# Performance work log

Hardware: AMD Instinct MI355X
Metric: run time of the kernel (lower is better)

Reference implementation:

```python
import jax, jax.numpy as jnp
import numpy as np
import math

V = 50000; E = 300; H = 512; T = 11; P = 18; L = 2048
NHEAD = 2; NLAYERS = 2; NUM_LSTM_LAYERS = 2; FF = E  # TransformerEncoderLayer dim_feedforward=embedding_dim
START, STOP = 0, 1
NEG = -10000.0


def _mk_lstm_params(key, in_dim, hid):
    ks = jax.random.split(key, 4)
    s = 1.0 / math.sqrt(hid)
    return {
        'Wi': jax.random.uniform(ks[0], (4 * hid, in_dim), minval=-s, maxval=s),
        'Wh': jax.random.uniform(ks[1], (4 * hid, hid), minval=-s, maxval=s),
        'bi': jax.random.uniform(ks[2], (4 * hid,), minval=-s, maxval=s),
        'bh': jax.random.uniform(ks[3], (4 * hid,), minval=-s, maxval=s),
    }


def setup_inputs() -> dict:
    key = jax.random.key(0)
    ks = jax.random.split(key, 32)
    sentence = jax.random.randint(ks[0], (L,), 0, V)
    pos_tagging = jax.random.randint(ks[1], (L,), 0, P)
    tf_idf = jax.random.uniform(ks[2], (L,))
    tags = jax.random.randint(ks[3], (L,), 2, T)  # avoid START/STOP as gold tags

    word_embeds = jax.random.normal(ks[4], (V, E)) * 0.1

    in_dim = E + P + 1
    half = H // 2
    lstm = []
    ki = 5
    for layer in range(NUM_LSTM_LAYERS):
        d = in_dim if layer == 0 else H
        lstm.append({'fwd': _mk_lstm_params(ks[ki], d, half), 'bwd': _mk_lstm_params(ks[ki + 1], d, half)})
        ki += 2
    h0 = jax.random.normal(ks[ki], (2 * NUM_LSTM_LAYERS, half)); ki += 1
    c0 = jax.random.normal(ks[ki], (2 * NUM_LSTM_LAYERS, half)); ki += 1

    def dense(k, o, i):
        s = 1.0 / math.sqrt(i)
        k1, k2 = jax.random.split(k)
        return (jax.random.uniform(k1, (o, i), minval=-s, maxval=s),
                jax.random.uniform(k2, (o,), minval=-s, maxval=s))

    tlayers = []
    for _ in range(NLAYERS):
        kk = jax.random.split(ks[ki], 8); ki += 1
        Wqkv, bqkv = dense(kk[0], 3 * H, H)
        Wo, bo = dense(kk[1], H, H)
        W1, b1 = dense(kk[2], FF, H)
        W2, b2 = dense(kk[3], H, FF)
        tlayers.append({
            'Wqkv': Wqkv, 'bqkv': bqkv, 'Wo': Wo, 'bo': bo,
            'W1': W1, 'b1': b1, 'W2': W2, 'b2': b2,
            'g1': jnp.ones((H,)), 'be1': jnp.zeros((H,)),
            'g2': jnp.ones((H,)), 'be2': jnp.zeros((H,)),
        })

    W_tag, b_tag = dense(ks[ki], T, H); ki += 1
    transitions = jax.random.normal(ks[ki], (T, T))
    transitions = transitions.at[START, :].set(NEG).at[:, STOP].set(NEG)

    # flatten transformer params into named entries
    inp = {
        'sentence': sentence, 'pos_tagging': pos_tagging, 'tf_idf': tf_idf, 'tags': tags,
        'word_embeds': word_embeds, 'h0': h0, 'c0': c0,
        'W_tag': W_tag, 'b_tag': b_tag, 'transitions': transitions,
    }
    for li in range(NUM_LSTM_LAYERS):
        for d in ('fwd', 'bwd'):
            for p in ('Wi', 'Wh', 'bi', 'bh'):
                inp[f'lstm{li}_{d}_{p}'] = lstm[li][d][p]
    for li in range(NLAYERS):
        for p, v in tlayers[li].items():
            inp[f't{li}_{p}'] = v
    return inp


def _lstm_dir(x, p, h0, c0, reverse):
    # x: [L, in_dim]
    def step(carry, xt):
        h, c = carry
        g = p['Wi'] @ xt + p['bi'] + p['Wh'] @ h + p['bh']
        i, f, gg, o = jnp.split(g, 4)
        i = jax.nn.sigmoid(i); f = jax.nn.sigmoid(f); o = jax.nn.sigmoid(o)
        c = f * c + i * jnp.tanh(gg)
        h = o * jnp.tanh(c)
        return (h, c), h
    _, hs = jax.lax.scan(step, (h0, c0), x, reverse=reverse)
    return hs  # [L, hid]


def _layernorm(x, g, b):
    m = jnp.mean(x, -1, keepdims=True)
    v = jnp.var(x, -1, keepdims=True)
    return (x - m) / jnp.sqrt(v + 1e-5) * g + b


def _pos_encoding(d_model, max_len):
    position = jnp.arange(max_len, dtype=jnp.float32)[:, None]
    div = jnp.exp(jnp.arange(0, d_model, 2, dtype=jnp.float32) * (-math.log(10000.0) / d_model))
    pe = jnp.zeros((max_len, d_model))
    pe = pe.at[:, 0::2].set(jnp.sin(position * div))
    pe = pe.at[:, 1::2].set(jnp.cos(position * div))
    return pe


def _encoder_layer(x, p, mask):
    # x: [L, H]; post-norm, relu FFN (PyTorch defaults), dropout=eval off
    Lx = x.shape[0]
    qkv = x @ p['Wqkv'].T + p['bqkv']
    q, k, v = jnp.split(qkv, 3, axis=-1)
    dh = H // NHEAD
    q = q.reshape(Lx, NHEAD, dh).transpose(1, 0, 2)
    k = k.reshape(Lx, NHEAD, dh).transpose(1, 0, 2)
    v = v.reshape(Lx, NHEAD, dh).transpose(1, 0, 2)
    scores = jnp.einsum('hqd,hkd->hqk', q, k) / math.sqrt(dh) + mask[None]
    attn = jax.nn.softmax(scores, axis=-1)
    o = jnp.einsum('hqk,hkd->hqd', attn, v).transpose(1, 0, 2).reshape(Lx, H)
    o = o @ p['Wo'].T + p['bo']
    x = _layernorm(x + o, p['g1'], p['be1'])
    ff = jax.nn.relu(x @ p['W1'].T + p['b1']) @ p['W2'].T + p['b2']
    return _layernorm(x + ff, p['g2'], p['be2'])


def _crf_forward(feats, transitions):
    # feats: [L, T]
    init = jnp.full((T,), NEG).at[START].set(0.0)
    def step(fv, feat):
        # next_tag_var[next, prev] = fv[prev] + trans[next, prev] + feat[next]
        m = fv[None, :] + transitions + feat[:, None]
        return jax.nn.logsumexp(m, axis=1), None
    fv, _ = jax.lax.scan(step, init, feats)
    return jax.nn.logsumexp(fv + transitions[STOP])


def _gold_score(feats, tags, transitions):
    ext = jnp.concatenate([jnp.array([START]), tags])
    Lx = feats.shape[0]
    emit = feats[jnp.arange(Lx), ext[1:]].sum()
    trans = transitions[ext[1:], ext[:-1]].sum()
    return emit + trans + transitions[STOP, ext[-1]]


def _forward_feats(sentence, pos_tagging, tf_idf, params):
    Lx = sentence.shape[0]
    embeds = params['word_embeds'][sentence]
    pos = jax.nn.one_hot(pos_tagging, P)
    x = jnp.concatenate([embeds, pos, tf_idf[:, None]], axis=1)  # [L, E+P+1]
    for li in range(NUM_LSTM_LAYERS):
        pf = {k: params[f'lstm{li}_fwd_{k}'] for k in ('Wi', 'Wh', 'bi', 'bh')}
        pb = {k: params[f'lstm{li}_bwd_{k}'] for k in ('Wi', 'Wh', 'bi', 'bh')}
        hf = _lstm_dir(x, pf, params['h0'][2 * li], params['c0'][2 * li], False)
        hb = _lstm_dir(x, pb, params['h0'][2 * li + 1], params['c0'][2 * li + 1], True)
        x = jnp.concatenate([hf, hb], axis=-1)  # [L, H]
    lstm_out = x
    src = lstm_out * math.sqrt(H) + _pos_encoding(H, Lx)
    mask = jnp.where(jnp.tril(jnp.ones((Lx, Lx), bool)), 0.0, -jnp.inf)
    for li in range(NLAYERS):
        p = {k: params[f't{li}_{k}'] for k in ('Wqkv', 'bqkv', 'Wo', 'bo', 'W1', 'b1', 'W2', 'b2', 'g1', 'be1', 'g2', 'be2')}
        src = _encoder_layer(src, p, mask)
    return src @ params['W_tag'].T + params['b_tag']  # [L, T]


def reference(sentence, pos_tagging, tf_idf, tags, word_embeds, h0, c0, W_tag, b_tag, transitions, **params):
    params = dict(params, word_embeds=word_embeds, h0=h0, c0=c0, W_tag=W_tag, b_tag=b_tag)
    feats = _forward_feats(sentence, pos_tagging, tf_idf, params)
    fwd = _crf_forward(feats, transitions)
    gold = _gold_score(feats, tags, transitions)
    return fwd - gold  # neg_log_likelihood scalar
```

## Files before the change

### kernel.cpp

```cpp
#include <hip/hip_runtime.h>
#include <math.h>

typedef unsigned short u16;
typedef unsigned int u32;
typedef _Float16 f16;
typedef f16 f16x2 __attribute__((ext_vector_type(2)));
typedef f16 f16x8 __attribute__((ext_vector_type(8)));
typedef short short8 __attribute__((ext_vector_type(8)));
typedef float f32x4 __attribute__((ext_vector_type(4)));

#define LSEQ 2048
#define NTAG 11

static __device__ __forceinline__ float b2f(u16 u){ union{u32 i; float f;} v; v.i=((u32)u)<<16; return v.f; }
static __device__ __forceinline__ u16 f2b(float f){ union{float fl; u32 i;} v; v.fl=f; u32 r=v.i+0x7fffu+((v.i>>16)&1u); return (u16)(r>>16); }
static u16 h_f2b(float f){ union{float fl; u32 i;} v; v.fl=f; u32 r=v.i+0x7fffu+((v.i>>16)&1u); return (u16)(r>>16); }
static __device__ __forceinline__ float tanh_f(float x){ float e=__expf(2.f*x); return 1.f - 2.f/(e+1.f); }
static __device__ __forceinline__ int dot4(u32 a, u32 b, int c){
#if __has_builtin(__builtin_amdgcn_sdot4)
  return __builtin_amdgcn_sdot4((int)a, (int)b, c, false);
#else
  int r = c;
  #pragma unroll
  for (int i=0;i<4;i++){
    int ai = (int)(a << (24-8*i)) >> 24;
    int bi = (int)(b << (24-8*i)) >> 24;
    r += ai*bi;
  }
  return r;
#endif
}

__global__ __launch_bounds__(256) void cvt2d_k(const float* __restrict__ src, u16* __restrict__ dst,
                                               int rows, int cols, int sld, int dld){
  int i = blockIdx.x*256 + threadIdx.x;
  if (i >= rows*dld) return;
  int r = i/dld, c = i - r*dld;
  float v = (c < cols) ? src[(long)r*sld + c] : 0.f;
  dst[i] = f2b(v);
}

__global__ __launch_bounds__(256) void whq_k(const float* __restrict__ wh,
                                             signed char* __restrict__ wq, float* __restrict__ srow){
  int row = blockIdx.x, j = threadIdx.x;
  float w = wh[row*256 + j];
  float a = fabsf(w);
  __shared__ float rm[4];
  int lane = j&63, wv = j>>6;
  #pragma unroll
  for (int o=32;o;o>>=1) a = fmaxf(a, __shfl_xor(a,o));
  if (!lane) rm[wv] = a;
  __syncthreads();
  float mx = fmaxf(fmaxf(rm[0],rm[1]),fmaxf(rm[2],rm[3]));
  float s = (mx > 0.f) ? mx*(1.f/127.f) : 1.f;
  int q = (int)rintf(w/s);
  q = q>127?127:(q<-127?-127:q);
  wq[((long)(j>>4)*1024 + row)*16 + (j&15)] = (signed char)q;
  if (j==0) srow[row] = s;
}

__global__ __launch_bounds__(256) void bsum_k(float* __restrict__ out,
    const float* bi0, const float* bh0, const float* bi1, const float* bh1,
    const float* bi2, const float* bh2, const float* bi3, const float* bh3){
  int i = blockIdx.x*256 + threadIdx.x;
  if (i >= 4096) return;
  int c = i>>10, j = i&1023;
  const float* bi = c==0?bi0:c==1?bi1:c==2?bi2:bi3;
  const float* bh = c==0?bh0:c==1?bh1:c==2?bh2:bh3;
  out[i] = bi[j] + bh[j];
}

__global__ void embed_k(const int* __restrict__ sent, const int* __restrict__ pos,
                        const float* __restrict__ tfidf, const float* __restrict__ we,
                        u16* __restrict__ x0h){
  int t = blockIdx.x, c = threadIdx.x;
  float v;
  if (c < 300)      v = we[(long)sent[t]*300 + c];
  else if (c < 318) v = (pos[t] == (c-300)) ? 1.f : 0.f;
  else if (c == 318) v = tfidf[t];
  else               v = 0.f;
  x0h[t*320 + c] = f2b(v);
}

__global__ __launch_bounds__(256) void gemm_k(const u16* __restrict__ A, const u16* __restrict__ B, void* __restrict__ C,
    int M, int N, int K, int lda, int ldb, int ldc,
    long aBS, long bBS, long cBS,
    const float* __restrict__ bias, int flags, int Npad)
{
  int zb = blockIdx.z;
  const u16* Ab = A + (long)zb*aBS;
  const u16* Bb = B + (long)zb*bBS;
  int m0 = blockIdx.y*64, n0 = blockIdx.x*64;
  __shared__ u16 As[64][40], Bs[64][40];
  int tid = threadIdx.x;
  int lane = tid & 63, wv = tid >> 6;
  int srow = tid >> 2, schk = tid & 3;
  int wr = wv >> 1, wc = wv & 1;
  int frow = lane & 15, fk = (lane >> 4) * 8;
  const u16* pa = Ab + (long)(m0+srow)*lda + schk*8;
  bool bval = (n0 + srow) < N;
  const u16* pb = Bb + (long)(n0+srow)*ldb + schk*8;
  f32x4 acc[2][2];
  #pragma unroll
  for (int mi=0;mi<2;mi++)
  #pragma unroll
  for (int ni=0;ni<2;ni++) acc[mi][ni] = (f32x4){0.f,0.f,0.f,0.f};

  for (int k0=0; k0<K; k0+=32){
    uint4 av = *(const uint4*)pa; pa += 32;
    uint4 bv; if (bval) bv = *(const uint4*)pb; else { bv.x=0u; bv.y=0u; bv.z=0u; bv.w=0u; }
    pb += 32;
    *(uint4*)&As[srow][schk*8] = av;
    *(uint4*)&Bs[srow][schk*8] = bv;
    __syncthreads();
    short8 a[2], b[2];
    a[0] = *(const short8*)&As[wr*32      + frow][fk];
    a[1] = *(const short8*)&As[wr*32 + 16 + frow][fk];
    b[0] = *(const short8*)&Bs[wc*32      + frow][fk];
    b[1] = *(const short8*)&Bs[wc*32 + 16 + frow][fk];
    #pragma unroll
    for (int mi=0;mi<2;mi++)
    #pragma unroll
    for (int ni=0;ni<2;ni++)
      acc[mi][ni] = __builtin_amdgcn_mfma_f32_16x16x32_bf16(a[mi], b[ni], acc[mi][ni], 0,0,0);
    __syncthreads();
  }
  int mrow = (lane>>4)*4, ncol = lane&15;
  #pragma unroll
  for (int mi=0;mi<2;mi++)
  #pragma unroll
  for (int ni=0;ni<2;ni++){
    int nn = n0 + wc*32 + ni*16 + ncol;
    #pragma unroll
    for (int j=0;j<4;j++){
      int mm = m0 + wr*32 + mi*16 + mrow + j;
      long ci = (long)zb*cBS + (long)mm*ldc + nn;
      if (nn < N){
        float v = acc[mi][ni][j];
        if (flags & 1) v += bias[nn];
        if (flags & 2) v = fmaxf(v, 0.f);
        if (flags & 4) ((u16*)C)[ci] = f2b(v); else ((float*)C)[ci] = v;
      } else if (nn < Npad){
        if (flags & 4) ((u16*)C)[ci] = 0; else ((float*)C)[ci] = 0.f;
      }
    }
  }
}

__global__ __launch_bounds__(1024) void lstm_r(
    const float* __restrict__ preF, const float* __restrict__ preB,
    const uint4* __restrict__ wqF, const uint4* __restrict__ wqB,
    const float* __restrict__ srF, const float* __restrict__ srB,
    const float* __restrict__ h0, const float* __restrict__ c0, int sbase,
    float* __restrict__ outf, u16* __restrict__ outh)
{
  int dir = blockIdx.x;
  const float* pre = dir ? preB : preF;
  const uint4* wq  = dir ? wqB  : wqF;
  float sr = (dir ? srB : srF)[threadIdx.x];
  __shared__ __align__(16) uint4 hl4[16];
  __shared__ float gl[1024];
  __shared__ float shv;
  __shared__ float rm[4];
  int tid = threadIdx.x;

  uint4 w[16];
  #pragma unroll
  for (int c=0;c<16;c++) w[c] = wq[c*1024 + tid];
  #pragma unroll
  for (int c=0;c<16;c++)
    asm volatile("" : "+v"(w[c].x), "+v"(w[c].y), "+v"(w[c].z), "+v"(w[c].w));

  float cst = 0.f, hinit = 0.f;
  if (tid < 256){
    hinit = h0[(sbase+dir)*256 + tid];
    cst   = c0[(sbase+dir)*256 + tid];
    float a = fabsf(hinit);
    int lane = tid&63, wv = tid>>6;
    #pragma unroll
    for (int o=32;o;o>>=1) a = fmaxf(a, __shfl_xor(a,o));
    if (!lane) rm[wv] = a;
  }
  __syncthreads();
  if (tid < 256){
    float mx = fmaxf(fmaxf(rm[0],rm[1]),fmaxf(rm[2],rm[3]));
    float sh = (mx > 1e-20f) ? mx*(1.f/127.f) : 1.f;
    int q = (int)rintf(hinit/sh);
    q = q>127?127:(q<-127?-127:q);
    ((signed char*)hl4)[tid] = (signed char)q;
    if (tid==0) shv = sh;
  }
  __syncthreads();

  for (int s=0; s<LSEQ; s++){
    int t = dir ? (LSEQ-1-s) : s;
    float pv = pre[(long)t*1024 + tid];
    float scale = sr * shv;
    int a0=0, a1=0, a2=0, a3=0;
    #pragma unroll
    for (int c=0;c<16;c++){
      uint4 hv = hl4[c];
      a0 = dot4(w[c].x, hv.x, a0);
      a1 = dot4(w[c].y, hv.y, a1);
      a2 = dot4(w[c].z, hv.z, a2);
      a3 = dot4(w[c].w, hv.w, a3);
    }
    gl[tid] = pv + scale*(float)((a0+a1)+(a2+a3));
    __syncthreads();
    if (tid < 256){
      float gi=gl[tid], gf=gl[tid+256], gg=gl[tid+512], go=gl[tid+768];
      float ii=1.f/(1.f+__expf(-gi));
      float ff=1.f/(1.f+__expf(-gf));
      float oo=1.f/(1.f+__expf(-go));
      cst = ff*cst + ii*tanh_f(gg);
      float h = oo*tanh_f(cst);
      long oi = (long)t*512 + dir*256 + tid;
      outf[oi] = h; outh[oi] = f2b(h);
      int q = (int)rintf(h*127.f);
      ((signed char*)hl4)[tid] = (signed char)q;
      if (tid==0) shv = 1.f/127.f;
    }
    __syncthreads();
  }
}

__global__ __launch_bounds__(512) void posenc_k(const float* __restrict__ xin, float* __restrict__ srcf, u16* __restrict__ srch){
  int t = blockIdx.x, d = threadIdx.x;
  long i = (long)t*512 + d;
  float v = xin[i] * 22.627416997969522f;
  float dv = __expf(-(float)(d & ~1) * 0.017988946039015984f);
  float ang = (float)t * dv;
  v += (d & 1) ? __cosf(ang) : __sinf(ang);
  srcf[i] = v; srch[i] = f2b(v);
}

__global__ __launch_bounds__(512) void trv_k(const u16* __restrict__ qkv, u16* __restrict__ vt){
  __shared__ u16 tile[64][65];
  int h = blockIdx.z;
  int lb = blockIdx.x*64, db = blockIdx.y*64;
  int tx = threadIdx.x, ty = threadIdx.y;
  #pragma unroll
  for (int j=0;j<8;j++){
    int l = lb + ty + j*8;
    tile[ty + j*8][tx] = qkv[(long)l*1536 + 1024 + h*256 + db + tx];
  }
  __syncthreads();
  #pragma unroll
  for (int j=0;j<8;j++){
    int d = db + ty + j*8;
    vt[((long)h*256 + d)*2048 + lb + tx] = tile[tx][ty + j*8];
  }
}

__global__ __launch_bounds__(256) void softmax_k(const float* __restrict__ sc, u16* __restrict__ P){
  int q = blockIdx.x;
  const float* row = sc + (long)q*LSEQ;
  u16* prow = P + (long)q*LSEQ;
  int tid = threadIdx.x, lane = tid&63, wv = tid>>6;
  int n = q + 1;
  __shared__ float sm[4], ss[4];
  __shared__ float ex[LSEQ];
  float mx = -1e30f;
  for (int c=tid; c<n; c+=256) mx = fmaxf(mx, row[c]);
  #pragma unroll
  for (int o=32;o;o>>=1) mx = fmaxf(mx, __shfl_xor(mx,o));
  if (!lane) sm[wv] = mx;
  __syncthreads();
  float mxs = fmaxf(fmaxf(sm[0],sm[1]),fmaxf(sm[2],sm[3])) * 0.0625f;
  float sum = 0.f;
  for (int c=tid; c<n; c+=256){
    float e = __expf(row[c]*0.0625f - mxs);
    ex[c] = e; sum += e;
  }
  #pragma unroll
  for (int o=32;o;o>>=1) sum += __shfl_xor(sum,o);
  if (!lane) ss[wv] = sum;
  __syncthreads();
  float inv = 1.f/(ss[0]+ss[1]+ss[2]+ss[3]);
  for (int c=tid; c<LSEQ; c+=256)
    prow[c] = (c<n) ? f2b(ex[c]*inv) : (u16)0;
}

__global__ __launch_bounds__(256) void addln_k(const float* __restrict__ x, const float* __restrict__ y,
                                               const float* __restrict__ g, const float* __restrict__ be,
                                               float* __restrict__ outf, u16* __restrict__ outh){
  int t = blockIdx.x, tid = threadIdx.x, lane = tid&63, wv = tid>>6;
  long base = (long)t*512;
  float v0 = x[base+tid]     + y[base+tid];
  float v1 = x[base+256+tid] + y[base+256+tid];
  float s = v0+v1, qq = v0*v0 + v1*v1;
  __shared__ float rs[4], rq[4];
  #pragma unroll
  for (int o=32;o;o>>=1){ s += __shfl_xor(s,o); qq += __shfl_xor(qq,o); }
  if (!lane){ rs[wv]=s; rq[wv]=qq; }
  __syncthreads();
  s  = rs[0]+rs[1]+rs[2]+rs[3];
  qq = rq[0]+rq[1]+rq[2]+rq[3];
  float mean = s*(1.f/512.f);
  float var  = qq*(1.f/512.f) - mean*mean;
  float inv = rsqrtf(var + 1e-5f);
  float o0 = (v0-mean)*inv*g[tid]     + be[tid];
  float o1 = (v1-mean)*inv*g[tid+256] + be[tid+256];
  outf[base+tid]     = o0; outh[base+tid]     = f2b(o0);
  outf[base+256+tid] = o1; outh[base+256+tid] = f2b(o1);
}

__global__ __launch_bounds__(256) void crf_k(const float* __restrict__ feats, const float* __restrict__ trans,
                                             const int* __restrict__ tags, u32* __restrict__ out){
  __shared__ float red[256];
  int tid = threadIdx.x;
  float acc = 0.f;
  for (int t=tid; t<LSEQ; t+=256){
    int tg = tags[t];
    int pv = t ? tags[t-1] : 0;
    acc += feats[t*NTAG + tg] + trans[tg*NTAG + pv];
  }
  red[tid] = acc; __syncthreads();
  for (int s=128; s; s>>=1){ if (tid < s) red[tid] += red[tid+s]; __syncthreads(); }
  float gold = red[0] + trans[1*NTAG + tags[LSEQ-1]];
  if (tid >= 64) return;
  int n = tid;
  bool act = n < NTAG;
  float Trow[NTAG];
  #pragma unroll
  for (int p=0;p<NTAG;p++) Trow[p] = act ? trans[n*NTAG + p] : 0.f;
  float fv = (n==0) ? 0.f : -10000.f;
  float feat = act ? feats[n] : 0.f;
  for (int t=0; t<LSEQ; t++){
    float featN = (t+1 < LSEQ) ? (act ? feats[(t+1)*NTAG + n] : 0.f) : 0.f;
    float v[NTAG]; float mx = -1e30f;
    #pragma unroll
    for (int p=0;p<NTAG;p++){
      float fvp = __shfl(fv, p);
      v[p] = fvp + Trow[p];
      mx = fmaxf(mx, v[p]);
    }
    float sum = 0.f;
    #pragma unroll
    for (int p=0;p<NTAG;p++) sum += __expf(v[p] - mx);
    fv = feat + mx + __logf(sum);
    feat = featN;
  }
  float tv = act ? fv + trans[1*NTAG + n] : -1e30f;
  float m2 = tv;
  #pragma unroll
  for (int o=32;o;o>>=1) m2 = fmaxf(m2, __shfl_xor(m2,o));
  float se = __expf(tv - m2);
  #pragma unroll
  for (int o=32;o;o>>=1) se += __shfl_xor(se,o);
  float fwd = m2 + __logf(se);
  if (tid == 0){
    u32 bits = (u32)f2b(fwd - gold);
    out[0] = (bits << 16) | bits;
  }
}

extern "C" void kernel_launch(void* const* d_in, const int* in_sizes, int n_in,
                              void* d_out, int out_size, void* d_ws, size_t ws_size,
                              hipStream_t stream) {
  (void)in_sizes; (void)n_in; (void)out_size;
  const int*   sent  = (const int*)  d_in[0];
  const int*   pos   = (const int*)  d_in[1];
  const float* tfidf = (const float*)d_in[2];
  const int*   tags  = (const int*)  d_in[3];
  const float* we    = (const float*)d_in[4];
  const float* h0    = (const float*)d_in[5];
  const float* c0    = (const float*)d_in[6];
  const float* Wtag  = (const float*)d_in[7];
  const float* btag  = (const float*)d_in[8];
  const float* trans = (const float*)d_in[9];
  const float* lWi[4] = {(const float*)d_in[10],(const float*)d_in[14],(const float*)d_in[18],(const float*)d_in[22]};
  const float* lWh[4] = {(const float*)d_in[11],(const float*)d_in[15],(const float*)d_in[19],(const float*)d_in[23]};
  const float* lbi[4] = {(const float*)d_in[12],(const float*)d_in[16],(const float*)d_in[20],(const float*)d_in[24]};
  const float* lbh[4] = {(const float*)d_in[13],(const float*)d_in[17],(const float*)d_in[21],(const float*)d_in[25]};
  const float *Wqkv[2], *bqkv[2], *Wo[2], *bo[2], *W1[2], *b1[2], *W2[2], *b2[2], *g1[2], *be1[2], *g2[2], *be2[2];
  for (int li=0; li<2; li++){
    const float** slots[12] = {&Wqkv[li],&bqkv[li],&Wo[li],&bo[li],&W1[li],&b1[li],&W2[li],&b2[li],&g1[li],&be1[li],&g2[li],&be2[li]};
    for (int k=0;k<12;k++) *slots[k] = (const float*)d_in[26 + li*12 + k];
  }

  auto wdiag = [&](float v){
    u16 u = h_f2b(v);
    unsigned char b0 = (unsigned char)(u & 0xFF), b1 = (unsigned char)(u >> 8);
    char* p = (char*)d_out;
    (void)hipMemsetAsync(p+0, b0, 1, stream);
    (void)hipMemsetAsync(p+1, b1, 1, stream);
    (void)hipMemsetAsync(p+2, b0, 1, stream);
    (void)hipMemsetAsync(p+3, b1, 1, stream);
  };
  (void)hipGetLastError();

  char* base = (char*)d_ws; size_t off = 0;
  auto alc = [&](size_t bytes)->char*{ char* p = base + off; off = (off + bytes + 255) & ~(size_t)255; return p; };

  u16* Wi0fH = (u16*)alc((size_t)1024*320*2);
  u16* Wi0bH = (u16*)alc((size_t)1024*320*2);
  u16* Wi1fH = (u16*)alc((size_t)1024*512*2);
  u16* Wi1bH = (u16*)alc((size_t)1024*512*2);
  u16* WqkvH[2] = {(u16*)alc((size_t)1536*512*2), (u16*)alc((size_t)1536*512*2)};
  u16* WoH[2]   = {(u16*)alc((size_t)512*512*2),  (u16*)alc((size_t)512*512*2)};
  u16* W1H[2]   = {(u16*)alc((size_t)300*512*2),  (u16*)alc((size_t)300*512*2)};
  u16* W2H[2]   = {(u16*)alc((size_t)512*320*2),  (u16*)alc((size_t)512*320*2)};
  u16* WtagH    = (u16*)alc((size_t)11*512*2);
  signed char* wqs[4]; float* srows[4];
  for (int c=0;c<4;c++) wqs[c] = (signed char*)alc((size_t)1024*256);
  for (int c=0;c<4;c++) srows[c] = (float*)alc((size_t)1024*4);
  float* bsums = (float*)alc((size_t)4*1024*4);
  u16* x0h = (u16*)alc((size_t)2048*320*2);
  float* preF = (float*)alc((size_t)2048*1024*4);
  float* preB = (float*)alc((size_t)2048*1024*4);
  float* scoresF = preF;
  float* xaf = (float*)alc((size_t)2048*512*4);
  u16*   xah = (u16*)  alc((size_t)2048*512*2);
  float* xbf = (float*)alc((size_t)2048*512*4);
  u16*   xbh = (u16*)  alc((size_t)2048*512*2);
  float* srcf = (float*)alc((size_t)2048*512*4);
  u16*   srch = (u16*)  alc((size_t)2048*512*2);
  u16* qkvh = (u16*)alc((size_t)2048*1536*2);
  u16* vth  = (u16*)alc((size_t)512*2048*2);
  u16* Pb   = (u16*)alc((size_t)2*2048*2048*2);
  u16* aoh  = (u16*)alc((size_t)2048*512*2);
  float* tmpf = (float*)alc((size_t)2048*512*4);
  u16* ff1h = (u16*)alc((size_t)2048*320*2);
  float* feats = (float*)alc((size_t)2048*NTAG*4);

  if (off > ws_size){ wdiag(-999.0f); return; }

  auto chk = [&](int stage)->bool{
    hipError_t e = hipGetLastError();
    if (e != hipSuccess){ wdiag(-(float)(stage*1000 + ((int)e % 1000))); return false; }
    return true;
  };

  auto cvt = [&](const float* s, u16* d, int r, int c, int sld, int dld){
    cvt2d_k<<<(r*dld+255)/256, 256, 0, stream>>>(s, d, r, c, sld, dld);
  };
  auto gemm = [&](const u16* A, const u16* B, void* C, int M, int N, int K,
                  int lda, int ldb, int ldc, long aBS, long bBS, long cBS,
                  const float* bias, int flags, int batch){
    dim3 g(((unsigned)N+63)/64, ((unsigned)M+63)/64, batch);
    gemm_k<<<g, 256, 0, stream>>>(A, B, C, M, N, K, lda, ldb, ldc, aBS, bBS, cBS, bias, flags, N);
  };

  cvt(lWi[0], Wi0fH, 1024, 319, 319, 320);
  cvt(lWi[1], Wi0bH, 1024, 319, 319, 320);
  cvt(lWi[2], Wi1fH, 1024, 512, 512, 512);
  cvt(lWi[3], Wi1bH, 1024, 512, 512, 512);
  for (int li=0; li<2; li++){
    cvt(Wqkv[li], WqkvH[li], 1536, 512, 512, 512);
    cvt(Wo[li],   WoH[li],   512, 512, 512, 512);
    cvt(W1[li],   W1H[li],   300, 512, 512, 512);
    cvt(W2[li],   W2H[li],   512, 300, 300, 320);
  }
  cvt(Wtag, WtagH, 11, 512, 512, 512);
  for (int c=0;c<4;c++) whq_k<<<1024, 256, 0, stream>>>(lWh[c], wqs[c], srows[c]);
  bsum_k<<<16, 256, 0, stream>>>(bsums, lbi[0],lbh[0], lbi[1],lbh[1], lbi[2],lbh[2], lbi[3],lbh[3]);
  embed_k<<<2048, 320, 0, stream>>>(sent, pos, tfidf, we, x0h);
  if (!chk(1)) return;

  gemm(x0h, Wi0fH, preF, 2048, 1024, 320, 320, 320, 1024, 0,0,0, bsums + 0,    1, 1);
  gemm(x0h, Wi0bH, preB, 2048, 1024, 320, 320, 320, 1024, 0,0,0, bsums + 1024, 1, 1);
  if (!chk(2)) return;
  lstm_r<<<2, 1024, 0, stream>>>(preF, preB, (const uint4*)wqs[0], (const uint4*)wqs[1],
                                 srows[0], srows[1], h0, c0, 0, xaf, xah);
  if (!chk(3)) return;

  gemm(xah, Wi1fH, preF, 2048, 1024, 512, 512, 512, 1024, 0,0,0, bsums + 2048, 1, 1);
  gemm(xah, Wi1bH, preB, 2048, 1024, 512, 512, 512, 1024, 0,0,0, bsums + 3072, 1, 1);
  lstm_r<<<2, 1024, 0, stream>>>(preF, preB, (const uint4*)wqs[2], (const uint4*)wqs[3],
                                 srows[2], srows[3], h0, c0, 2, xbf, xbh);
  if (!chk(4)) return;

  posenc_k<<<2048, 512, 0, stream>>>(xbf, srcf, srch);
  if (!chk(5)) return;

  for (int li=0; li<2; li++){
    gemm(srch, WqkvH[li], qkvh, 2048, 1536, 512, 512, 512, 1536, 0,0,0, bqkv[li], 1|4, 1);
    trv_k<<<dim3(32,4,2), dim3(64,8), 0, stream>>>(qkvh, vth);
    for (int h=0; h<2; h++){
      gemm(qkvh + h*256, qkvh + 512 + h*256, scoresF, 2048, 2048, 256, 1536, 1536, 2048, 0,0,0, nullptr, 0, 1);
      softmax_k<<<2048, 256, 0, stream>>>(scoresF, Pb + (long)h*2048*2048);
    }
    gemm(Pb, vth, aoh, 2048, 256, 2048, 2048, 2048, 512,
         (long)2048*2048, (long)256*2048, 256, nullptr, 4, 2);
    gemm(aoh, WoH[li], tmpf, 2048, 512, 512, 512, 512, 512, 0,0,0, bo[li], 1, 1);
    addln_k<<<2048, 256, 0, stream>>>(srcf, tmpf, g1[li], be1[li], srcf, srch);
    gemm(srch, W1H[li], ff1h, 2048, 300, 512, 512, 512, 320, 0,0,0, b1[li], 1|2|4, 1);
    gemm(ff1h, W2H[li], tmpf, 2048, 512, 320, 320, 320, 512, 0,0,0, b2[li], 1, 1);
    addln_k<<<2048, 256, 0, stream>>>(srcf, tmpf, g2[li], be2[li], srcf, srch);
    if (!chk(6 + li)) return;
  }

  gemm(srch, WtagH, feats, 2048, NTAG, 512, 512, 512, NTAG, 0,0,0, btag, 1, 1);
  crf_k<<<1, 256, 0, stream>>>(feats, trans, tags, (u32*)d_out);
  if (!chk(8)) return;
}
```

Baseline: 5.888 ms.

## Interleave LSTM gate rows so gates combine via lane shuffles with one barrier

Permutes the quantized recurrent weight rows so each hidden unit's four gates land in four adjacent threads. Gates are exchanged with warp shuffles, removing the shared gate buffer and one barrier per timestep. The hidden state is double-buffered in shared memory. Weights are now reloaded from global memory every step rather than kept in registers, which adds cache traffic on the serial path.

```diff
diff --git a/kernel.cpp b/kernel.cpp
--- a/kernel.cpp
+++ b/kernel.cpp
@@ -42,8 +42,8 @@
 
 __global__ __launch_bounds__(256) void whq_k(const float* __restrict__ wh,
                                              signed char* __restrict__ wq, float* __restrict__ srow){
-  int row = blockIdx.x, j = threadIdx.x;
-  float w = wh[row*256 + j];
+  int r = blockIdx.x, j = threadIdx.x;
+  float w = wh[r*256 + j];
   float a = fabsf(w);
   __shared__ float rm[4];
   int lane = j&63, wv = j>>6;
@@ -55,8 +55,9 @@
   float s = (mx > 0.f) ? mx*(1.f/127.f) : 1.f;
   int q = (int)rintf(w/s);
   q = q>127?127:(q<-127?-127:q);
-  wq[((long)(j>>4)*1024 + row)*16 + (j&15)] = (signed char)q;
-  if (j==0) srow[row] = s;
+  int p = 4*(r & 255) + (r >> 8);
+  wq[((long)(j>>4)*1024 + p)*16 + (j&15)] = (signed char)q;
+  if (j==0) srow[p] = s;
 }
 
 __global__ __launch_bounds__(256) void bsum_k(float* __restrict__ out,
@@ -147,7 +148,7 @@
   }
 }
 
-__global__ __launch_bounds__(1024) void lstm_r(
+__global__ __launch_bounds__(1024) void lstm_s(
     const float* __restrict__ preF, const float* __restrict__ preB,
     const uint4* __restrict__ wqF, const uint4* __restrict__ wqB,
     const float* __restrict__ srF, const float* __restrict__ srB,
@@ -158,67 +159,68 @@
   const float* pre = dir ? preB : preF;
   const uint4* wq  = dir ? wqB  : wqF;
   float sr = (dir ? srB : srF)[threadIdx.x];
-  __shared__ __align__(16) uint4 hl4[16];
-  __shared__ float gl[1024];
-  __shared__ float shv;
-  __shared__ float rm[4];
+  __shared__ __align__(16) signed char hlb[2][256];
+  __shared__ float rm[16];
   int tid = threadIdx.x;
-
-  uint4 w[16];
-  #pragma unroll
-  for (int c=0;c<16;c++) w[c] = wq[c*1024 + tid];
-  #pragma unroll
-  for (int c=0;c<16;c++)
-    asm volatile("" : "+v"(w[c].x), "+v"(w[c].y), "+v"(w[c].z), "+v"(w[c].w));
-
-  float cst = 0.f, hinit = 0.f;
-  if (tid < 256){
-    hinit = h0[(sbase+dir)*256 + tid];
-    cst   = c0[(sbase+dir)*256 + tid];
-    float a = fabsf(hinit);
-    int lane = tid&63, wv = tid>>6;
-    #pragma unroll
-    for (int o=32;o;o>>=1) a = fmaxf(a, __shfl_xor(a,o));
-    if (!lane) rm[wv] = a;
-  }
-  __syncthreads();
-  if (tid < 256){
-    float mx = fmaxf(fmaxf(rm[0],rm[1]),fmaxf(rm[2],rm[3]));
-    float sh = (mx > 1e-20f) ? mx*(1.f/127.f) : 1.f;
-    int q = (int)rintf(hinit/sh);
+  int g = tid & 3, u = tid >> 2;
+  int lane = tid & 63, wvi = tid >> 6;
+
+  float cst = c0[(sbase+dir)*256 + u];
+  float hi  = h0[(sbase+dir)*256 + u];
+  float a = fabsf(hi);
+  #pragma unroll
+  for (int o=32;o;o>>=1) a = fmaxf(a, __shfl_xor(a,o));
+  if (!lane) rm[wvi] = a;
+  __syncthreads();
+  float mx = 0.f;
+  #pragma unroll
+  for (int i=0;i<16;i++) mx = fmaxf(mx, rm[i]);
+  float sh0 = (mx > 1e-20f) ? mx*(1.f/127.f) : 1.f;
+  if (g == 0){
+    int q = (int)rintf(hi/sh0);
     q = q>127?127:(q<-127?-127:q);
-    ((signed char*)hl4)[tid] = (signed char)q;
-    if (tid==0) shv = sh;
-  }
-  __syncthreads();
-
+    hlb[0][u] = (signed char)q;
+  }
+  __syncthreads();
+
+  const float c127 = 1.f/127.f;
   for (int s=0; s<LSEQ; s++){
     int t = dir ? (LSEQ-1-s) : s;
-    float pv = pre[(long)t*1024 + tid];
-    float scale = sr * shv;
+    float pv = pre[(long)t*1024 + g*256 + u];
+    float scale = sr * ((s==0) ? sh0 : c127);
+    int rb = s & 1, wb = rb ^ 1;
+    uint4 w[16];
+    #pragma unroll
+    for (int c=0;c<16;c++) w[c] = wq[c*1024 + tid];
+    #pragma unroll
+    for (int c=0;c<16;c++)
+      asm volatile("" : "+v"(w[c].x), "+v"(w[c].y), "+v"(w[c].z), "+v"(w[c].w));
     int a0=0, a1=0, a2=0, a3=0;
     #pragma unroll
     for (int c=0;c<16;c++){
-      uint4 hv = hl4[c];
+      uint4 hv = *(const uint4*)&hlb[rb][c*16];
       a0 = dot4(w[c].x, hv.x, a0);
       a1 = dot4(w[c].y, hv.y, a1);
       a2 = dot4(w[c].z, hv.z, a2);
       a3 = dot4(w[c].w, hv.w, a3);
     }
-    gl[tid] = pv + scale*(float)((a0+a1)+(a2+a3));
-    __syncthreads();
-    if (tid < 256){
-      float gi=gl[tid], gf=gl[tid+256], gg=gl[tid+512], go=gl[tid+768];
-      float ii=1.f/(1.f+__expf(-gi));
-      float ff=1.f/(1.f+__expf(-gf));
-      float oo=1.f/(1.f+__expf(-go));
-      cst = ff*cst + ii*tanh_f(gg);
-      float h = oo*tanh_f(cst);
-      long oi = (long)t*512 + dir*256 + tid;
+    float val = pv + scale*(float)((a0+a1)+(a2+a3));
+    float x1 = __shfl_xor(val, 1);
+    float x2 = __shfl_xor(val, 2);
+    float x3 = __shfl_xor(x1, 2);
+    float gi = (g==0)?val:(g==1)?x1:(g==2)?x2:x3;
+    float gf = (g==0)?x1:(g==1)?val:(g==2)?x3:x2;
+    float gg = (g==0)?x2:(g==1)?x3:(g==2)?val:x1;
+    float go = (g==0)?x3:(g==1)?x2:(g==2)?x1:val;
+    float ii = 1.f/(1.f+__expf(-gi));
+    float ff = 1.f/(1.f+__expf(-gf));
+    float oo = 1.f/(1.f+__expf(-go));
+    cst = ff*cst + ii*tanh_f(gg);
+    float h = oo*tanh_f(cst);
+    if (g == 0){
+      long oi = (long)t*512 + dir*256 + u;
       outf[oi] = h; outh[oi] = f2b(h);
-      int q = (int)rintf(h*127.f);
-      ((signed char*)hl4)[tid] = (signed char)q;
-      if (tid==0) shv = 1.f/127.f;
+      hlb[wb][u] = (signed char)(int)rintf(h*127.f);
     }
     __syncthreads();
   }
@@ -461,13 +463,13 @@
   gemm(x0h, Wi0fH, preF, 2048, 1024, 320, 320, 320, 1024, 0,0,0, bsums + 0,    1, 1);
   gemm(x0h, Wi0bH, preB, 2048, 1024, 320, 320, 320, 1024, 0,0,0, bsums + 1024, 1, 1);
   if (!chk(2)) return;
-  lstm_r<<<2, 1024, 0, stream>>>(preF, preB, (const uint4*)wqs[0], (const uint4*)wqs[1],
+  lstm_s<<<2, 1024, 0, stream>>>(preF, preB, (const uint4*)wqs[0], (const uint4*)wqs[1],
                                  srows[0], srows[1], h0, c0, 0, xaf, xah);
   if (!chk(3)) return;
 
   gemm(xah, Wi1fH, preF, 2048, 1024, 512, 512, 512, 1024, 0,0,0, bsums + 2048, 1, 1);
   gemm(xah, Wi1bH, preB, 2048, 1024, 512, 512, 512, 1024, 0,0,0, bsums + 3072, 1, 1);
-  lstm_r<<<2, 1024, 0, stream>>>(preF, preB, (const uint4*)wqs[2], (const uint4*)wqs[3],
+  lstm_s<<<2, 1024, 0, stream>>>(preF, preB, (const uint4*)wqs[2], (const uint4*)wqs[3],
                                  srows[2], srows[3], h0, c0, 2, xbf, xbh);
   if (!chk(4)) return;
 
```

Result: slower. 14.76 ms (+150.7%).
